# Optimization experiments

Hardware: AMD Instinct MI355X
Metric: run time of the kernel (lower is better)

## Reference

```python
import jax, jax.numpy as jnp
import numpy as np

CUBE = (80, 80, 20)
NBINS = CUBE[0] * CUBE[1] * CUBE[2]  # 128000
NVIEW = 5
B = 2
C_IMG, C_FEAT = 3, 32
H_IMG, W_IMG = 512, 512
H_F, W_F = 128, 128
HID = 256
IN_DIM = 3 + 2 * (C_IMG + C_FEAT)  # 73


def setup_inputs() -> dict:
    key = jax.random.key(0)
    ks = jax.random.split(key, 8)
    denorm_imgs = jax.random.uniform(ks[0], (NVIEW, B, C_IMG, H_IMG, W_IMG), jnp.float32)
    feats2d = jax.random.normal(ks[1], (NVIEW, B, C_FEAT, H_F, W_F), jnp.float32)
    # grid_sample coords in [-1, 1], last dim = (x, y)
    sample_grid = jax.random.uniform(ks[2], (NVIEW, NBINS, 2), jnp.float32, -1.0, 1.0)
    points = jax.random.normal(ks[3], (NBINS, 3), jnp.float32)
    W1 = jax.random.normal(ks[4], (IN_DIM, HID), jnp.float32) * (1.0 / np.sqrt(IN_DIM))
    b1 = jnp.zeros((HID,), jnp.float32)
    W2 = jax.random.normal(ks[5], (HID, 1), jnp.float32) * (1.0 / np.sqrt(HID))
    b2 = jnp.zeros((1,), jnp.float32)
    return {"denorm_imgs": denorm_imgs, "feats2d": feats2d, "sample_grid": sample_grid,
            "points": points, "W1": W1, "b1": b1, "W2": W2, "b2": b2}


def _grid_sample(img, grid):
    """Bilinear grid_sample, align_corners=True, padding_mode='zeros'.
    img: [B, C, H, W]; grid: [N, 2] in [-1, 1] (x, y). Returns [B, C, N]."""
    H, W = img.shape[-2], img.shape[-1]
    ix = (grid[:, 0] + 1.0) * 0.5 * (W - 1)
    iy = (grid[:, 1] + 1.0) * 0.5 * (H - 1)
    x0 = jnp.floor(ix)
    y0 = jnp.floor(iy)
    x1 = x0 + 1.0
    y1 = y0 + 1.0
    wx1 = ix - x0
    wx0 = 1.0 - wx1
    wy1 = iy - y0
    wy0 = 1.0 - wy1

    def corner(x, y, w):
        valid = ((x >= 0) & (x <= W - 1) & (y >= 0) & (y <= H - 1)).astype(img.dtype)
        xi = jnp.clip(x, 0, W - 1).astype(jnp.int32)
        yi = jnp.clip(y, 0, H - 1).astype(jnp.int32)
        vals = img[:, :, yi, xi]  # [B, C, N]
        return vals * (w * valid)[None, None, :]

    return (corner(x0, y0, wx0 * wy0) + corner(x1, y0, wx1 * wy0)
            + corner(x0, y1, wx0 * wy1) + corner(x1, y1, wx1 * wy1))


def reference(denorm_imgs, feats2d, sample_grid, points, W1, b1, W2, b2):
    # Batched multi-view grid_sample: [V, B, C, N]
    cubes_img = jax.vmap(_grid_sample)(denorm_imgs, sample_grid)
    cubes_feat = jax.vmap(_grid_sample)(feats2d, sample_grid)
    cubes = jnp.concatenate([cubes_img, cubes_feat], axis=2)  # [V, B, C_tot, N]
    cubes = jnp.transpose(cubes, (1, 2, 3, 0))  # [B, C_tot, N, V]
    nview = cubes.shape[-1]
    mean = jnp.sum(cubes, axis=-1, keepdims=True) / nview          # [B, C, N, 1]
    var = jnp.sum((cubes - mean) ** 2, axis=-1, keepdims=True) / nview
    var = jnp.exp(-var)
    gvol = jnp.concatenate([mean[..., 0], var[..., 0]], axis=1)    # [B, 2C, N]
    feats = jnp.transpose(gvol, (0, 2, 1))                         # [B, N, 2C]
    bsz = feats.shape[0]
    pts = jnp.broadcast_to(points[None], (bsz,) + points.shape)    # [B, N, 3]
    inp = jnp.concatenate([pts, feats], axis=-1)                   # [B, N, 3+2C]
    h = jax.nn.relu(inp @ W1 + b1)
    density = jax.nn.softplus(h @ W2 + b2)                         # [B, N, 1]
    alpha = 1.0 - jnp.exp(-density)
    return alpha.reshape(bsz, 1, CUBE[0], CUBE[1], CUBE[2])
```

## Files before the change

### kernel.cpp

```cpp
#include <hip/hip_runtime.h>

#define NVIEW 5
#define NB    128000
#define CF    32
#define HID   256
#define KA    96
#define IMG_HW 262144
#define FT_HW  16384

typedef __attribute__((ext_vector_type(8))) short short8;
typedef __attribute__((ext_vector_type(4))) float f32x4;

__device__ __forceinline__ unsigned int f2bf(float f) {
    unsigned int u = __float_as_uint(f);
    return (u + 0x7fffu + ((u >> 16) & 1u)) >> 16;
}
__device__ __forceinline__ unsigned int pk(float a, float b) {
    return f2bf(a) | (f2bf(b) << 16);
}
__device__ __forceinline__ float b2f_lo(unsigned int u) { return __uint_as_float(u << 16); }
__device__ __forceinline__ float b2f_hi(unsigned int u) { return __uint_as_float(u & 0xffff0000u); }

__device__ __forceinline__ int mapk(int k) {
    if (k < 22) return k;
    if (k < 25) return k + 16;
    if (k == 25) return -1;
    if (k < 42) return k + 15;
    if (k < 48) return -1;
    if (k < 64) return k - 26;
    if (k < 80) return k - 7;
    return -1;
}

__global__ __launch_bounds__(256) void prep(
    const float* __restrict__ imgs, const float* __restrict__ feats,
    const float* __restrict__ W1, const float* __restrict__ b1,
    const float* __restrict__ W2, const float* __restrict__ b2,
    uint2* __restrict__ imgsP, uint4* __restrict__ featsP,
    unsigned int* __restrict__ Bfrag, float* __restrict__ bw)
{
    const int bidx = blockIdx.x;
    const int t = threadIdx.x;
    if (bidx < 1280) {
        int gid = bidx * 256 + t;
        int v   = gid >> 16;
        int px  = (gid & 65535) * 4;
        const float* base = imgs + (size_t)v * 6 * IMG_HW + px;
        float4 pl[6];
        #pragma unroll
        for (int p = 0; p < 6; p++)
            pl[p] = *(const float4*)(base + (size_t)p * IMG_HW);
        uint2 o[4];
        #pragma unroll
        for (int i = 0; i < 4; i++) {
            unsigned int c[6];
            #pragma unroll
            for (int p = 0; p < 6; p++)
                c[p] = (unsigned int)fminf(((const float*)&pl[p])[i] * 255.f + 0.5f, 255.f);
            o[i].x = c[0] | (c[1] << 8) | (c[2] << 16);
            o[i].y = c[3] | (c[4] << 8) | (c[5] << 16);
        }
        uint4* dst = (uint4*)(imgsP + (size_t)v * IMG_HW + px);
        dst[0] = make_uint4(o[0].x, o[0].y, o[1].x, o[1].y);
        dst[1] = make_uint4(o[2].x, o[2].y, o[3].x, o[3].y);
    } else if (bidx < 2560) {
        __shared__ unsigned short tile[64][65];
        const int pixbase = (bidx - 1280) * 64;
        const int v   = pixbase >> 14;
        const int rem = pixbase & 16383;
        {
            const int p = t & 63;
            const int s = t >> 6;
            #pragma unroll
            for (int it = 0; it < 16; it++) {
                int plane = it * 4 + s;
                tile[plane][p] =
                    (unsigned short)f2bf(feats[((size_t)v * 64 + plane) * FT_HW + rem + p]);
            }
        }
        __syncthreads();
        {
            const int q = t & 7;
            #pragma unroll
            for (int it = 0; it < 2; it++) {
                int p = it * 32 + (t >> 3);
                uint4 o;
                o.x = (unsigned)tile[q * 8 + 0][p] | ((unsigned)tile[q * 8 + 1][p] << 16);
                o.y = (unsigned)tile[q * 8 + 2][p] | ((unsigned)tile[q * 8 + 3][p] << 16);
                o.z = (unsigned)tile[q * 8 + 4][p] | ((unsigned)tile[q * 8 + 5][p] << 16);
                o.w = (unsigned)tile[q * 8 + 6][p] | ((unsigned)tile[q * 8 + 7][p] << 16);
                featsP[(size_t)(pixbase + p) * 8 + q] = o;
            }
        }
    } else {
        int e = (bidx - 2560) * 256 + t;
        int ju = e & 3;
        int nn = (e >> 2) & 255;
        int o  = e >> 10;
        int k0 = o * 8 + ju * 2;
        int i0 = mapk(k0), i1 = mapk(k0 + 1);
        float f0 = (i0 >= 0) ? W1[i0 * 256 + nn] : 0.f;
        float f1 = (i1 >= 0) ? W1[i1 * 256 + nn] : 0.f;
        Bfrag[e] = pk(f0, f1);
        if (e < 256)       bw[e] = b1[e];
        else if (e < 512)  bw[e] = W2[e - 256];
        else if (e == 512) bw[e] = b2[0];
    }
}

#define AROW 13

__global__ __launch_bounds__(256, 2) void fused_gather_mlp(
    const uint2* __restrict__ imgsP,
    const unsigned short* __restrict__ featsP,
    const float* __restrict__ grid,
    const float* __restrict__ points,
    const unsigned int*   __restrict__ Bfrag,
    const float*          __restrict__ bw,
    float* __restrict__ out)
{
    __shared__ unsigned int Bl[3072];
    __shared__ uint4 As4[128 * AROW];

    const int tid = threadIdx.x;

    {
        const uint4* src = (const uint4*)Bfrag;
        uint4* dst = (uint4*)Bl;
        #pragma unroll
        for (int i = 0; i < 3; i++) {
            int f  = i * 256 + tid;
            int o  = f >> 6;
            int wi = f & 63;
            dst[f] = src[o * 256 + wi];
        }
    }
    const float b2v = bw[512];

    const int n    = blockIdx.x * 64 + (tid >> 2);
    const int b    = (tid >> 1) & 1;
    const int half = tid & 1;

    float sumf[16], ssqf[16];
    #pragma unroll
    for (int c = 0; c < 16; c++) { sumf[c] = 0.f; ssqf[c] = 0.f; }
    float si0 = 0.f, si1 = 0.f, si2 = 0.f;
    float qi0 = 0.f, qi1 = 0.f, qi2 = 0.f;
    float p0 = 0.f, p1 = 0.f, p2 = 0.f;
    if (half == 0) {
        p0 = points[n * 3 + 0];
        p1 = points[n * 3 + 1];
        p2 = points[n * 3 + 2];
    }

    #pragma unroll
    for (int v = 0; v < NVIEW; v++) {
        const float2 g = ((const float2*)grid)[v * NB + n];
        const float gx = g.x, gy = g.y;

        if (half == 0) {
            float ix = (gx + 1.f) * 0.5f * 511.f;
            float iy = (gy + 1.f) * 0.5f * 511.f;
            float x0f = floorf(ix), y0f = floorf(iy);
            float x1f = x0f + 1.f, y1f = y0f + 1.f;
            float wx1 = ix - x0f, wx0 = 1.f - wx1;
            float wy1 = iy - y0f, wy0 = 1.f - wy1;
            float vi0 = 0.f, vi1 = 0.f, vi2 = 0.f;
            const uint2* base = imgsP + (size_t)v * IMG_HW;
            #pragma unroll
            for (int k = 0; k < 4; k++) {
                float xf = (k & 1) ? x1f : x0f;
                float yf = (k >> 1) ? y1f : y0f;
                float w  = ((k & 1) ? wx1 : wx0) * ((k >> 1) ? wy1 : wy0);
                float vd = (xf >= 0.f && xf <= 511.f && yf >= 0.f && yf <= 511.f) ? 1.f : 0.f;
                w *= vd;
                int xi = (int)fminf(fmaxf(xf, 0.f), 511.f);
                int yi = (int)fminf(fmaxf(yf, 0.f), 511.f);
                uint2 iv = base[yi * 512 + xi];
                unsigned int sel = b ? iv.y : iv.x;
                vi0 += w * (float)(sel & 255u);
                vi1 += w * (float)((sel >> 8) & 255u);
                vi2 += w * (float)((sel >> 16) & 255u);
            }
            si0 += vi0; qi0 += vi0 * vi0;
            si1 += vi1; qi1 += vi1 * vi1;
            si2 += vi2; qi2 += vi2 * vi2;
        }

        {
            float ix = (gx + 1.f) * 0.5f * 127.f;
            float iy = (gy + 1.f) * 0.5f * 127.f;
            float x0f = floorf(ix), y0f = floorf(iy);
            float x1f = x0f + 1.f, y1f = y0f + 1.f;
            float wx1 = ix - x0f, wx0 = 1.f - wx1;
            float wy1 = iy - y0f, wy0 = 1.f - wy1;
            const unsigned short* fb =
                featsP + ((size_t)v * FT_HW) * 64 + b * 32 + half * 16;
            float val[16];
            #pragma unroll
            for (int c = 0; c < 16; c++) val[c] = 0.f;
            #pragma unroll
            for (int k = 0; k < 4; k++) {
                float xf = (k & 1) ? x1f : x0f;
                float yf = (k >> 1) ? y1f : y0f;
                float w  = ((k & 1) ? wx1 : wx0) * ((k >> 1) ? wy1 : wy0);
                float vd = (xf >= 0.f && xf <= 127.f && yf >= 0.f && yf <= 127.f) ? 1.f : 0.f;
                w *= vd;
                int xi = (int)fminf(fmaxf(xf, 0.f), 127.f);
                int yi = (int)fminf(fmaxf(yf, 0.f), 127.f);
                const uint4* p = (const uint4*)(fb + (size_t)(yi * 128 + xi) * 64);
                #pragma unroll
                for (int q = 0; q < 2; q++) {
                    uint4 f4 = p[q];
                    val[q * 8 + 0] += w * b2f_lo(f4.x);
                    val[q * 8 + 1] += w * b2f_hi(f4.x);
                    val[q * 8 + 2] += w * b2f_lo(f4.y);
                    val[q * 8 + 3] += w * b2f_hi(f4.y);
                    val[q * 8 + 4] += w * b2f_lo(f4.z);
                    val[q * 8 + 5] += w * b2f_hi(f4.z);
                    val[q * 8 + 6] += w * b2f_lo(f4.w);
                    val[q * 8 + 7] += w * b2f_hi(f4.w);
                }
            }
            #pragma unroll
            for (int c = 0; c < 16; c++) {
                sumf[c] += val[c];
                ssqf[c] += val[c] * val[c];
            }
        }
    }

    #pragma unroll
    for (int c = 0; c < 16; c++) {
        float m = sumf[c] * 0.2f;
        float q = ssqf[c] * 0.2f - m * m;
        sumf[c] = m;
        ssqf[c] = expf(-q);
    }
    const float s1 = 0.2f * (1.f / 255.f);
    const float s2 = 0.2f * (1.f / 65025.f);
    float mi0 = si0 * s1, mi1 = si1 * s1, mi2 = si2 * s1;
    float ei0 = expf(-(qi0 * s2 - mi0 * mi0));
    float ei1 = expf(-(qi1 * s2 - mi1 * mi1));
    float ei2 = expf(-(qi2 * s2 - mi2 * mi2));

    unsigned int u[24];
    if (half == 0) {
        u[0] = pk(p0, p1);
        u[1] = pk(p2, mi0);
        u[2] = pk(mi1, mi2);
        #pragma unroll
        for (int j = 0; j < 8; j++) u[3 + j] = pk(sumf[2 * j], sumf[2 * j + 1]);
        u[11] = pk(ei0, ei1);
        u[12] = pk(ei2, 0.f);
        #pragma unroll
        for (int j = 0; j < 8; j++) u[13 + j] = pk(ssqf[2 * j], ssqf[2 * j + 1]);
        u[21] = 0u; u[22] = 0u; u[23] = 0u;
    } else {
        #pragma unroll
        for (int j = 0; j < 8; j++) u[j]     = pk(sumf[2 * j], sumf[2 * j + 1]);
        #pragma unroll
        for (int j = 0; j < 8; j++) u[8 + j] = pk(ssqf[2 * j], ssqf[2 * j + 1]);
        #pragma unroll
        for (int j = 16; j < 24; j++) u[j] = 0u;
    }

    {
        uint4* arow = &As4[(tid >> 1) * AROW + half * 6];
        #pragma unroll
        for (int i = 0; i < 6; i++)
            arow[i] = make_uint4(u[4 * i], u[4 * i + 1], u[4 * i + 2], u[4 * i + 3]);
    }
    __syncthreads();

    const int w    = tid >> 6;
    const int lane = tid & 63;
    const int col  = lane & 15;
    const int quad = lane >> 4;
    const long rowbase = (long)blockIdx.x * 128 + w * 32;

    short8 af[2][3];
    #pragma unroll
    for (int s = 0; s < 3; s++) {
        af[0][s] = *(const short8*)&As4[(w * 32 + col)      * AROW + s * 4 + quad];
        af[1][s] = *(const short8*)&As4[(w * 32 + 16 + col) * AROW + s * 4 + quad];
    }

    float pm[2][4] = {{0.f, 0.f, 0.f, 0.f}, {0.f, 0.f, 0.f, 0.f}};
    for (int qd = 0; qd < 4; qd++) {
        if (qd > 0) {
            __syncthreads();
            const uint4* src = (const uint4*)Bfrag;
            uint4* dst = (uint4*)Bl;
            #pragma unroll
            for (int i = 0; i < 3; i++) {
                int f  = i * 256 + tid;
                int o  = f >> 6;
                int wi = f & 63;
                dst[f] = src[o * 256 + qd * 64 + wi];
            }
            __syncthreads();
        }

        f32x4 acc[2][4];
        #pragma unroll
        for (int m = 0; m < 2; m++)
            #pragma unroll
            for (int t = 0; t < 4; t++)
                acc[m][t] = (f32x4){0.f, 0.f, 0.f, 0.f};

        #pragma unroll
        for (int s = 0; s < 3; s++) {
            #pragma unroll
            for (int t = 0; t < 4; t++) {
                short8 bf = *(const short8*)(Bl + (s * 4 + quad) * 256 + (t * 16 + col) * 4);
                acc[0][t] = __builtin_amdgcn_mfma_f32_16x16x32_bf16(af[0][s], bf, acc[0][t], 0, 0, 0);
                acc[1][t] = __builtin_amdgcn_mfma_f32_16x16x32_bf16(af[1][s], bf, acc[1][t], 0, 0, 0);
            }
        }

        #pragma unroll
        for (int t = 0; t < 4; t++) {
            int j = qd * 64 + t * 16 + col;
            float b1v = bw[j];
            float w2v = bw[256 + j];
            #pragma unroll
            for (int m = 0; m < 2; m++)
                #pragma unroll
                for (int r = 0; r < 4; r++) {
                    float hh = fmaxf(acc[m][t][r] + b1v, 0.f);
                    pm[m][r] += hh * w2v;
                }
        }
    }

    #pragma unroll
    for (int m = 0; m < 2; m++)
        #pragma unroll
        for (int r = 0; r < 4; r++) {
            float p = pm[m][r];
            p += __shfl_xor(p, 1);
            p += __shfl_xor(p, 2);
            p += __shfl_xor(p, 4);
            p += __shfl_xor(p, 8);
            pm[m][r] = p;
        }

    if (col == 0) {
        #pragma unroll
        for (int m = 0; m < 2; m++)
            #pragma unroll
            for (int r = 0; r < 4; r++) {
                float x  = pm[m][r] + b2v;
                float sp = fmaxf(x, 0.f) + log1pf(expf(-fabsf(x)));
                float alpha = -expm1f(-sp);
                long row = rowbase + m * 16 + quad * 4 + r;
                out[(row & 1) * (long)NB + (row >> 1)] = alpha;
            }
    }
}

extern "C" void kernel_launch(void* const* d_in, const int* in_sizes, int n_in,
                              void* d_out, int out_size, void* d_ws, size_t ws_size,
                              hipStream_t stream) {
    const float* imgs   = (const float*)d_in[0];
    const float* feats  = (const float*)d_in[1];
    const float* grid   = (const float*)d_in[2];
    const float* points = (const float*)d_in[3];
    const float* W1     = (const float*)d_in[4];
    const float* b1     = (const float*)d_in[5];
    const float* W2     = (const float*)d_in[6];
    const float* b2     = (const float*)d_in[7];
    float* out = (float*)d_out;

    uint2*          imgsP  = (uint2*)d_ws;
    unsigned short* featsP = (unsigned short*)(imgsP + (size_t)NVIEW * IMG_HW);
    unsigned int*   Bfrag  = (unsigned int*)(featsP + (size_t)NVIEW * FT_HW * 64);
    float*          bwbuf  = (float*)(Bfrag + 12288);

    prep<<<dim3(2608), dim3(256), 0, stream>>>(
        imgs, feats, W1, b1, W2, b2,
        imgsP, (uint4*)featsP, Bfrag, bwbuf);
    fused_gather_mlp<<<dim3(2000), dim3(256), 0, stream>>>(
        imgsP, featsP, grid, points, Bfrag, bwbuf, out);
}
```

Before: 189.9 us.

## Stage full W1 fragment in LDS once and compute all hidden units in one pass

The kernel now loads the whole bf16 W1 fragment (48 KB) plus b1 and W2 into shared memory once per block. This removes the four-chunk loop that reloaded a quarter of the weights and issued two barriers per chunk. The MFMA loop then accumulates all 256 hidden columns at once, using 128 accumulator registers per lane. The cost is much higher LDS use and register pressure, which can lower occupancy under the launch bound of 2 blocks per SIMD.

```diff
diff --git a/kernel.cpp b/kernel.cpp
--- a/kernel.cpp
+++ b/kernel.cpp
@@ -119,8 +119,10 @@
     const float*          __restrict__ bw,
     float* __restrict__ out)
 {
-    __shared__ unsigned int Bl[3072];
+    __shared__ unsigned int Bl[12288];
     __shared__ uint4 As4[128 * AROW];
+    __shared__ float b1s[HID];
+    __shared__ float W2s[HID];
 
     const int tid = threadIdx.x;
 
@@ -128,12 +130,9 @@
         const uint4* src = (const uint4*)Bfrag;
         uint4* dst = (uint4*)Bl;
         #pragma unroll
-        for (int i = 0; i < 3; i++) {
-            int f  = i * 256 + tid;
-            int o  = f >> 6;
-            int wi = f & 63;
-            dst[f] = src[o * 256 + wi];
-        }
+        for (int i = 0; i < 12; i++) dst[i * 256 + tid] = src[i * 256 + tid];
+        b1s[tid] = bw[tid];
+        W2s[tid] = bw[256 + tid];
     }
     const float b2v = bw[512];
 
@@ -279,61 +278,40 @@
     const int quad = lane >> 4;
     const long rowbase = (long)blockIdx.x * 128 + w * 32;
 
-    short8 af[2][3];
+    f32x4 acc[2][16];
+    #pragma unroll
+    for (int m = 0; m < 2; m++)
+        #pragma unroll
+        for (int t = 0; t < 16; t++)
+            acc[m][t] = (f32x4){0.f, 0.f, 0.f, 0.f};
+
+    const unsigned int* bp = Bl + (quad * 256 + col) * 4;
+
     #pragma unroll
     for (int s = 0; s < 3; s++) {
-        af[0][s] = *(const short8*)&As4[(w * 32 + col)      * AROW + s * 4 + quad];
-        af[1][s] = *(const short8*)&As4[(w * 32 + 16 + col) * AROW + s * 4 + quad];
+        short8 af0 = *(const short8*)&As4[(w * 32 + col)      * AROW + s * 4 + quad];
+        short8 af1 = *(const short8*)&As4[(w * 32 + 16 + col) * AROW + s * 4 + quad];
+        #pragma unroll
+        for (int t = 0; t < 16; t++) {
+            short8 bf = *(const short8*)(bp + s * 4096 + t * 64);
+            acc[0][t] = __builtin_amdgcn_mfma_f32_16x16x32_bf16(af0, bf, acc[0][t], 0, 0, 0);
+            acc[1][t] = __builtin_amdgcn_mfma_f32_16x16x32_bf16(af1, bf, acc[1][t], 0, 0, 0);
+        }
     }
 
     float pm[2][4] = {{0.f, 0.f, 0.f, 0.f}, {0.f, 0.f, 0.f, 0.f}};
-    for (int qd = 0; qd < 4; qd++) {
-        if (qd > 0) {
-            __syncthreads();
-            const uint4* src = (const uint4*)Bfrag;
-            uint4* dst = (uint4*)Bl;
-            #pragma unroll
-            for (int i = 0; i < 3; i++) {
-                int f  = i * 256 + tid;
-                int o  = f >> 6;
-                int wi = f & 63;
-                dst[f] = src[o * 256 + qd * 64 + wi];
-            }
-            __syncthreads();
-        }
-
-        f32x4 acc[2][4];
+    #pragma unroll
+    for (int t = 0; t < 16; t++) {
+        float b1v = b1s[t * 16 + col];
+        float w2v = W2s[t * 16 + col];
         #pragma unroll
         for (int m = 0; m < 2; m++)
             #pragma unroll
-            for (int t = 0; t < 4; t++)
-                acc[m][t] = (f32x4){0.f, 0.f, 0.f, 0.f};
-
-        #pragma unroll
-        for (int s = 0; s < 3; s++) {
-            #pragma unroll
-            for (int t = 0; t < 4; t++) {
-                short8 bf = *(const short8*)(Bl + (s * 4 + quad) * 256 + (t * 16 + col) * 4);
-                acc[0][t] = __builtin_amdgcn_mfma_f32_16x16x32_bf16(af[0][s], bf, acc[0][t], 0, 0, 0);
-                acc[1][t] = __builtin_amdgcn_mfma_f32_16x16x32_bf16(af[1][s], bf, acc[1][t], 0, 0, 0);
-            }
-        }
-
-        #pragma unroll
-        for (int t = 0; t < 4; t++) {
-            int j = qd * 64 + t * 16 + col;
-            float b1v = bw[j];
-            float w2v = bw[256 + j];
-            #pragma unroll
-            for (int m = 0; m < 2; m++)
-                #pragma unroll
-                for (int r = 0; r < 4; r++) {
-                    float hh = fmaxf(acc[m][t][r] + b1v, 0.f);
-                    pm[m][r] += hh * w2v;
-                }
-        }
-    }
-
+            for (int r = 0; r < 4; r++) {
+                float h = fmaxf(acc[m][t][r] + b1v, 0.f);
+                pm[m][r] += h * w2v;
+            }
+    }
     #pragma unroll
     for (int m = 0; m < 2; m++)
         #pragma unroll
```

After: 190.2 us. About the same (+0.1%).
